# Optimization experiments

Hardware: AMD Instinct MI355X
Metric: run time of the kernel (lower is better)

Reference implementation:

```python
import jax, jax.numpy as jnp
import numpy as np

B = 512          # number of drug-combination graphs (batch)
MAX_LEN = 128    # static padding for to_dense_batch
D_DRUG = 256     # drug_in_features (kdim = vdim)
D_CELL = 1024    # cell_in_features
H = 16           # nheads
HD = 64          # h (per-head dim)
E = H * HD       # embed_dim = 1024


def setup_inputs() -> dict:
    key = jax.random.key(0)
    ks = jax.random.split(key, 12)
    N = 32768
    x_nodes = jax.random.normal(ks[0], (N, D_DRUG), dtype=jnp.float32)
    guide = jnp.sort(jax.random.randint(ks[1], (N,), 0, B)).astype(jnp.int64)
    cell = jax.random.normal(ks[2], (B, D_CELL), dtype=jnp.float32)
    s = 0.02
    return {
        "x_nodes": x_nodes,
        "cell": cell,
        "Wq": jax.random.normal(ks[3], (E, E), dtype=jnp.float32) * s,
        "bq": jnp.zeros((E,), dtype=jnp.float32),
        "Wk": jax.random.normal(ks[4], (E, D_DRUG), dtype=jnp.float32) * s,
        "bk": jnp.zeros((E,), dtype=jnp.float32),
        "Wv": jax.random.normal(ks[5], (E, D_DRUG), dtype=jnp.float32) * s,
        "bv": jnp.zeros((E,), dtype=jnp.float32),
        "Wo": jax.random.normal(ks[6], (E, E), dtype=jnp.float32) * s,
        "bo": jnp.zeros((E,), dtype=jnp.float32),
        "Wc": jax.random.normal(ks[7], (E, D_CELL), dtype=jnp.float32) * s,
        "bc": jnp.zeros((E,), dtype=jnp.float32),
        "guide": guide,
    }


def _to_dense_batch(x_nodes, guide):
    # Faithful torch_geometric.to_dense_batch with static MAX_LEN padding.
    N = x_nodes.shape[0]
    ones = jnp.ones((N,), dtype=jnp.int32)
    counts = jax.ops.segment_sum(ones, guide, num_segments=B)      # [B]
    starts = jnp.cumsum(counts) - counts                            # [B]
    pos = jnp.arange(N, dtype=jnp.int32) - starts[guide]            # rank within segment
    dense = jnp.zeros((B, MAX_LEN, x_nodes.shape[1]), x_nodes.dtype).at[guide, pos].set(x_nodes)
    mask = jnp.zeros((B, MAX_LEN), dtype=bool).at[guide, pos].set(True)
    return dense, mask


def reference(x_nodes, cell, Wq, bq, Wk, bk, Wv, bv, Wo, bo, Wc, bc, guide):
    drug_key, mask = _to_dense_batch(x_nodes, guide)                # [B,M,D_DRUG], [B,M]
    # cell_query_fc then MHA q-projection (single query per graph)
    cq = cell @ Wc.T + bc                                           # [B,E]
    q = (cq @ Wq.T + bq).reshape(B, H, HD) * (HD ** -0.5)           # [B,H,hd]
    k = (drug_key @ Wk.T + bk).reshape(B, MAX_LEN, H, HD)           # [B,M,H,hd]
    v = (drug_key @ Wv.T + bv).reshape(B, MAX_LEN, H, HD)
    scores = jnp.einsum('bhd,bmhd->bhm', q, k)                      # [B,H,M]
    scores = jnp.where(mask[:, None, :], scores, -1e9)
    attn = jax.nn.softmax(scores, axis=-1)
    out = jnp.einsum('bhm,bmhd->bhd', attn, v).reshape(B, E)        # [B,E]
    out = out @ Wo.T + bo
    return jnp.concatenate([out, cell], axis=1)                     # [B, E + D_CELL]
```

## Files before the change

### kernel.cpp

```cpp
#include <hip/hip_runtime.h>
#include <hip/hip_bf16.h>
#include <math.h>

#define B_GRAPHS 512
#define MAXLEN   128
#define DDRUG    256
#define NH       16
#define EMB      1024

typedef __attribute__((ext_vector_type(4))) float f32x4;
typedef __attribute__((ext_vector_type(8))) short s16x8;
typedef __attribute__((ext_vector_type(4))) short s16x4;

__device__ inline short f2bf(float f) {
    unsigned u = __builtin_bit_cast(unsigned, f);
    u += 0x7FFF + ((u >> 16) & 1);
    return (short)(u >> 16);
}
__device__ inline float bf2f(short s) {
    unsigned u = ((unsigned)(unsigned short)s) << 16;
    return __builtin_bit_cast(float, u);
}

__device__ inline void cvt4(const float* __restrict__ in, short* __restrict__ out, int j)
{
    f32x4 v = ((const f32x4*)in)[j];
    s16x4 o;
    o.x = f2bf(v.x); o.y = f2bf(v.y); o.z = f2bf(v.z); o.w = f2bf(v.w);
    ((s16x4*)out)[j] = o;
}

__global__ __launch_bounds__(256) void prep_kernel(
    const float* __restrict__ cell, const float* __restrict__ Wc,
    const float* __restrict__ Wq,   const float* __restrict__ Wo,
    const float* __restrict__ Wv,   const int* __restrict__ g32, int N,
    float* __restrict__ out, short* __restrict__ cell_bf, short* __restrict__ Wc_bf,
    short* __restrict__ Wq_bf, short* __restrict__ Wo_bf, short* __restrict__ Wv_bf,
    int* __restrict__ starts)
{
    const int stride = gridDim.x * 256;
    for (int i = blockIdx.x * 256 + threadIdx.x; i < 1114625; i += stride) {
        if      (i <  131072) cvt4(cell, cell_bf, i);
        else if (i <  393216) cvt4(Wc, Wc_bf, i - 131072);
        else if (i <  655360) cvt4(Wq, Wq_bf, i - 393216);
        else if (i <  917504) cvt4(Wo, Wo_bf, i - 655360);
        else if (i <  983040) cvt4(Wv, Wv_bf, i - 917504);
        else if (i < 1114112) {
            int j = i - 983040;
            int b = j >> 8, c4 = j & 255;
            *(f32x4*)&out[(size_t)b * 2048 + 1024 + c4 * 4] = ((const f32x4*)cell)[j];
        } else {
            int b = i - 1114112;
            bool is64 = (g32[N - 1] == 0);
            int lo = 0, hi = N;
            while (lo < hi) {
                int mid = (lo + hi) >> 1;
                int v = is64 ? g32[2 * mid] : g32[mid];
                if (v < b) lo = mid + 1; else hi = mid;
            }
            starts[b] = lo;
        }
    }
}

template<bool OUT_BF>
__global__ __launch_bounds__(256) void gemm32_bf16_nt(
    const short* __restrict__ A, int lda,
    const short* __restrict__ Bw, int ldb,
    const float* __restrict__ bias, void* __restrict__ Cout,
    int ldc, float scale, int K)
{
    __shared__ short As[32 * 64];
    __shared__ short Bs[32 * 64];
    const int t = threadIdx.x, lane = t & 63, w = t >> 6;
    const int wm = w >> 1, wn = w & 1;
    const int row0 = blockIdx.y * 32, col0 = blockIdx.x * 32;
    f32x4 c = {0.f, 0.f, 0.f, 0.f};

    const int sr = t >> 3, sc = (t & 7) * 8;
    const int swz = (sr & 7) << 4;

    for (int kt = 0; kt < K; kt += 64) {
        s16x8 va = *(const s16x8*)&A [(size_t)(row0 + sr) * lda + kt + sc];
        s16x8 vb = *(const s16x8*)&Bw[(size_t)(col0 + sr) * ldb + kt + sc];
        *(s16x8*)((char*)As + sr * 128 + ((sc * 2) ^ swz)) = va;
        *(s16x8*)((char*)Bs + sr * 128 + ((sc * 2) ^ swz)) = vb;
        __syncthreads();
        #pragma unroll
        for (int ks = 0; ks < 2; ++ks) {
            const int kk = (ks * 32 + (lane >> 4) * 8) * 2;
            int ra = wm * 16 + (lane & 15);
            s16x8 a = *(const s16x8*)((char*)As + ra * 128 + (kk ^ ((ra & 7) << 4)));
            int rb = wn * 16 + (lane & 15);
            s16x8 b = *(const s16x8*)((char*)Bs + rb * 128 + (kk ^ ((rb & 7) << 4)));
            c = __builtin_amdgcn_mfma_f32_16x16x32_bf16(a, b, c, 0, 0, 0);
        }
        __syncthreads();
    }
    const int m0 = row0 + wm * 16 + (lane >> 4) * 4;
    const int nn = col0 + wn * 16 + (lane & 15);
    #pragma unroll
    for (int r = 0; r < 4; ++r) {
        float v = (c[r] + bias[nn]) * scale;
        if (OUT_BF) ((short*)Cout)[(size_t)(m0 + r) * ldc + nn] = f2bf(v);
        else        ((float*)Cout)[(size_t)(m0 + r) * ldc + nn] = v;
    }
}

__global__ __launch_bounds__(256) void qk_kernel(
    const float* __restrict__ q, const float* __restrict__ Wk, short* __restrict__ qkout)
{
    __shared__ float q_s[8][64];
    const int bt = blockIdx.x, h = blockIdx.y, t = threadIdx.x;
    for (int i = t; i < 512; i += 256)
        q_s[i >> 6][i & 63] = q[(size_t)(bt * 8 + (i >> 6)) * EMB + h * 64 + (i & 63)];
    __syncthreads();
    float acc[8] = {};
    const float* wbase = &Wk[(size_t)h * 64 * DDRUG + t];
    #pragma unroll 4
    for (int j = 0; j < 64; ++j) {
        float wv = wbase[(size_t)j * DDRUG];
        #pragma unroll
        for (int bb = 0; bb < 8; ++bb) acc[bb] += q_s[bb][j] * wv;
    }
    #pragma unroll
    for (int bb = 0; bb < 8; ++bb)
        qkout[(size_t)(bt * 8 + bb) * 4096 + h * DDRUG + t] = f2bf(acc[bb]);
}

__global__ __launch_bounds__(256) void attn_kernel(
    const float* __restrict__ X, const short* __restrict__ qk,
    const int* __restrict__ starts, short* __restrict__ xbar, int Ntot)
{
    __shared__ short qk_s[8 * 256];
    __shared__ short Xs[64 * 256];
    __shared__ float S_s[128 * 12];
    const int b = blockIdx.x, half = blockIdx.y, t = threadIdx.x;
    const int lane = t & 63, w = t >> 6;
    const int s0 = starts[b];
    int n = starts[b + 1] - s0;
    if (n > MAXLEN) n = MAXLEN;

    {
        int hl = t >> 5, cc = (t & 31) * 8;
        const s16x8* src = (const s16x8*)(qk + (size_t)b * 4096 + (half * 8 + hl) * 256 + cc);
        *(s16x8*)((char*)qk_s + hl * 512 + ((cc * 2) ^ ((hl & 7) << 4))) = src[0];
    }

    const int sr = t >> 2, scg = (t & 3) * 64;
    auto stageX = [&](int st) {
        int gm = s0 + st * 64 + sr;
        if (gm > Ntot - 1) gm = Ntot - 1;
        const f32x4* src = (const f32x4*)(X + (size_t)gm * 256 + scg);
        int swzr = (sr & 7) << 4;
        #pragma unroll
        for (int j = 0; j < 8; ++j) {
            f32x4 a = src[2 * j], bb = src[2 * j + 1];
            s16x8 v;
            v[0] = f2bf(a.x);  v[1] = f2bf(a.y);  v[2] = f2bf(a.z);  v[3] = f2bf(a.w);
            v[4] = f2bf(bb.x); v[5] = f2bf(bb.y); v[6] = f2bf(bb.z); v[7] = f2bf(bb.w);
            *(s16x8*)((char*)Xs + sr * 512 + (((scg + j * 8) * 2) ^ swzr)) = v;
        }
    };
    stageX(0);
    __syncthreads();

    s16x8 af[8];
    {
        int r = lane & 7, swzh = r << 4;
        #pragma unroll
        for (int ks = 0; ks < 8; ++ks) {
            int k = ks * 32 + (lane >> 4) * 8;
            af[ks] = *(const s16x8*)((char*)qk_s + r * 512 + ((k * 2) ^ swzh));
        }
    }
    auto mfmaStage = [&](int st) {
        int lr = w * 16 + (lane & 15);
        int swzr = (lr & 7) << 4;
        f32x4 c = {0.f, 0.f, 0.f, 0.f};
        #pragma unroll
        for (int ks = 0; ks < 8; ++ks) {
            int k = ks * 32 + (lane >> 4) * 8;
            s16x8 bf = *(const s16x8*)((char*)Xs + lr * 512 + ((k * 2) ^ swzr));
            c = __builtin_amdgcn_mfma_f32_16x16x32_bf16(af[ks], bf, c, 0, 0, 0);
        }
        int m = st * 64 + w * 16 + (lane & 15);
        int hb = (lane >> 4) * 4;
        if (hb < 8) {
            #pragma unroll
            for (int i = 0; i < 4; ++i) S_s[m * 12 + hb + i] = c[i];
        }
    };
    mfmaStage(0);
    if (n > 64) {
        __syncthreads();
        stageX(1);
        __syncthreads();
        mfmaStage(1);
    }
    __syncthreads();

    #pragma unroll
    for (int hh = 0; hh < 2; ++hh) {
        int h = w * 2 + hh;
        float v0 = (lane < n)      ? S_s[lane * 12 + h]        : -INFINITY;
        float v1 = (lane + 64 < n) ? S_s[(lane + 64) * 12 + h] : -INFINITY;
        float mx = fmaxf(v0, v1);
        #pragma unroll
        for (int off = 32; off > 0; off >>= 1) mx = fmaxf(mx, __shfl_xor(mx, off, 64));
        float e0 = (lane < n)      ? __expf(v0 - mx) : 0.f;
        float e1 = (lane + 64 < n) ? __expf(v1 - mx) : 0.f;
        float sm = e0 + e1;
        #pragma unroll
        for (int off = 32; off > 0; off >>= 1) sm += __shfl_xor(sm, off, 64);
        float inv = 1.f / sm;
        if (lane < n)      S_s[lane * 12 + h]        = e0 * inv;
        if (lane + 64 < n) S_s[(lane + 64) * 12 + h] = e1 * inv;
    }
    __syncthreads();

    const int d = t;
    float acc[8] = {};
    const float* Xb = X + (size_t)s0 * 256 + d;
    int m = 0;
    for (; m + 4 <= n; m += 4) {
        float xv[4];
        #pragma unroll
        for (int u = 0; u < 4; ++u) xv[u] = Xb[(size_t)(m + u) * 256];
        #pragma unroll
        for (int u = 0; u < 4; ++u) {
            const f32x4* prow = (const f32x4*)&S_s[(m + u) * 12];
            f32x4 p0 = prow[0], p1 = prow[1];
            float x = xv[u];
            acc[0] += p0.x * x; acc[1] += p0.y * x; acc[2] += p0.z * x; acc[3] += p0.w * x;
            acc[4] += p1.x * x; acc[5] += p1.y * x; acc[6] += p1.z * x; acc[7] += p1.w * x;
        }
    }
    for (; m < n; ++m) {
        const f32x4* prow = (const f32x4*)&S_s[m * 12];
        f32x4 p0 = prow[0], p1 = prow[1];
        float x = Xb[(size_t)m * 256];
        acc[0] += p0.x * x; acc[1] += p0.y * x; acc[2] += p0.z * x; acc[3] += p0.w * x;
        acc[4] += p1.x * x; acc[5] += p1.y * x; acc[6] += p1.z * x; acc[7] += p1.w * x;
    }
    short* xb = xbar + (size_t)b * 4096 + (size_t)(half * 8) * 256 + d;
    #pragma unroll
    for (int h = 0; h < 8; ++h) xb[(size_t)h * 256] = f2bf(acc[h]);
}

__global__ __launch_bounds__(256) void outh_gemm(
    const short* __restrict__ xbar,
    const short* __restrict__ Wv_bf,
    const float* __restrict__ bv, short* __restrict__ outh)
{
    __shared__ short As[64 * 64];
    __shared__ short Bs[64 * 64];
    const int t = threadIdx.x, lane = t & 63, w = t >> 6;
    const int wm = w >> 1, wn = w & 1;
    const int h = blockIdx.y;
    const int row0 = blockIdx.x * 64;
    const short* A = xbar + (size_t)h * 256;
    const short* B = Wv_bf + (size_t)h * 64 * 256;
    f32x4 c[2][2] = {};

    const int sr = t >> 2, sc = (t & 3) * 16;
    const int swz = (sr & 7) << 4;
    const int kb0 = (lane >> 4) * 8;

    for (int kt = 0; kt < 256; kt += 64) {
        s16x8 va0 = *(const s16x8*)&A[(size_t)(row0 + sr) * 4096 + kt + sc];
        s16x8 va1 = *(const s16x8*)&A[(size_t)(row0 + sr) * 4096 + kt + sc + 8];
        s16x8 vb0 = *(const s16x8*)&B[(size_t)sr * 256 + kt + sc];
        s16x8 vb1 = *(const s16x8*)&B[(size_t)sr * 256 + kt + sc + 8];
        *(s16x8*)((char*)As + sr * 128 + ((sc * 2)      ^ swz)) = va0;
        *(s16x8*)((char*)As + sr * 128 + ((sc * 2 + 16) ^ swz)) = va1;
        *(s16x8*)((char*)Bs + sr * 128 + ((sc * 2)      ^ swz)) = vb0;
        *(s16x8*)((char*)Bs + sr * 128 + ((sc * 2 + 16) ^ swz)) = vb1;
        __syncthreads();
        #pragma unroll
        for (int ks = 0; ks < 2; ++ks) {
            const int kk = (ks * 32 + kb0) * 2;
            s16x8 a0, a1, b0, b1;
            {
                int r = wm * 32 + (lane & 15);
                a0 = *(const s16x8*)((char*)As + r * 128 + (kk ^ ((r & 7) << 4)));
                int r2 = r + 16;
                a1 = *(const s16x8*)((char*)As + r2 * 128 + (kk ^ ((r2 & 7) << 4)));
            }
            {
                int r = wn * 32 + (lane & 15);
                b0 = *(const s16x8*)((char*)Bs + r * 128 + (kk ^ ((r & 7) << 4)));
                int r2 = r + 16;
                b1 = *(const s16x8*)((char*)Bs + r2 * 128 + (kk ^ ((r2 & 7) << 4)));
            }
            c[0][0] = __builtin_amdgcn_mfma_f32_16x16x32_bf16(a0, b0, c[0][0], 0, 0, 0);
            c[0][1] = __builtin_amdgcn_mfma_f32_16x16x32_bf16(a0, b1, c[0][1], 0, 0, 0);
            c[1][0] = __builtin_amdgcn_mfma_f32_16x16x32_bf16(a1, b0, c[1][0], 0, 0, 0);
            c[1][1] = __builtin_amdgcn_mfma_f32_16x16x32_bf16(a1, b1, c[1][1], 0, 0, 0);
        }
        __syncthreads();
    }
    #pragma unroll
    for (int i = 0; i < 2; ++i)
    #pragma unroll
    for (int j = 0; j < 2; ++j) {
        int m0 = row0 + wm * 32 + i * 16 + (lane >> 4) * 4;
        int nn = wn * 32 + j * 16 + (lane & 15);
        #pragma unroll
        for (int r = 0; r < 4; ++r) {
            float v = c[i][j][r] + bv[h * 64 + nn];
            outh[(size_t)(m0 + r) * EMB + h * 64 + nn] = f2bf(v);
        }
    }
}

extern "C" void kernel_launch(void* const* d_in, const int* in_sizes, int n_in,
                              void* d_out, int out_size, void* d_ws, size_t ws_size,
                              hipStream_t stream)
{
    const float* x_nodes = (const float*)d_in[0];
    const float* cell    = (const float*)d_in[1];
    const float* Wq      = (const float*)d_in[2];
    const float* bq      = (const float*)d_in[3];
    const float* Wk      = (const float*)d_in[4];
    const float* Wv      = (const float*)d_in[6];
    const float* bv      = (const float*)d_in[7];
    const float* Wo      = (const float*)d_in[8];
    const float* bo      = (const float*)d_in[9];
    const float* Wc      = (const float*)d_in[10];
    const float* bc      = (const float*)d_in[11];
    const int*   guide   = (const int*)d_in[12];
    const int N = in_sizes[12];
    float* out = (float*)d_out;

    char* ws = (char*)d_ws;
    int*   starts  = (int*)ws;
    float* qf32    = (float*)(ws + 4096);
    short* cell_bf = (short*)(ws + 4096 + (2u << 20));
    short* cq_bf   = (short*)(ws + 4096 + (3u << 20));
    short* outh_bf = (short*)(ws + 4096 + (4u << 20));
    short* qk_bf   = (short*)(ws + 4096 + (5u << 20));
    short* xbar_bf = (short*)(ws + 4096 + (9u << 20));
    short* Wc_bf   = (short*)(ws + 4096 + (13u << 20));
    short* Wq_bf   = (short*)(ws + 4096 + (15u << 20));
    short* Wo_bf   = (short*)(ws + 4096 + (17u << 20));
    short* Wv_bf   = (short*)(ws + 4096 + (19u << 20));

    prep_kernel<<<2048, 256, 0, stream>>>(
        cell, Wc, Wq, Wo, Wv, guide, N, out,
        cell_bf, Wc_bf, Wq_bf, Wo_bf, Wv_bf, starts);

    gemm32_bf16_nt<true ><<<dim3(32, 16), 256, 0, stream>>>(
        cell_bf, 1024, Wc_bf, 1024, bc, cq_bf, 1024, 1.0f, 1024);
    gemm32_bf16_nt<false><<<dim3(32, 16), 256, 0, stream>>>(
        cq_bf, 1024, Wq_bf, 1024, bq, qf32, 1024, 0.125f, 1024);

    qk_kernel<<<dim3(B_GRAPHS / 8, NH), 256, 0, stream>>>(qf32, Wk, qk_bf);

    attn_kernel<<<dim3(B_GRAPHS, 2), 256, 0, stream>>>(x_nodes, qk_bf, starts, xbar_bf, N);

    outh_gemm<<<dim3(8, NH), 256, 0, stream>>>(xbar_bf, Wv_bf, bv, outh_bf);

    gemm32_bf16_nt<false><<<dim3(32, 16), 256, 0, stream>>>(
        outh_bf, 1024, Wo_bf, 1024, bo, out, 2048, 1.0f, 1024);

    (void)in_sizes; (void)n_in; (void)out_size; (void)ws_size;
}
```

Before: 181.4 us.

## Process all heads per graph block and reuse staged bf16 X for weighted sum

The attention kernel now handles all 16 heads in a single block per graph instead of splitting heads across two blocks. This halves the global reads of the fp32 node features X. The whole 128-row X tile is staged into shared memory as bf16, and the attention-weighted sum reads from that tile instead of re-reading fp32 X from global memory. In exchange the kernel uses more LDS (64KB X plus the score buffer), which lowers occupancy, launches half as many blocks, and now accumulates the weighted sum from bf16-rounded X.

```diff
diff --git a/kernel.cpp b/kernel.cpp
--- a/kernel.cpp
+++ b/kernel.cpp
@@ -132,24 +132,25 @@
     const float* __restrict__ X, const short* __restrict__ qk,
     const int* __restrict__ starts, short* __restrict__ xbar, int Ntot)
 {
-    __shared__ short qk_s[8 * 256];
-    __shared__ short Xs[64 * 256];
-    __shared__ float S_s[128 * 12];
-    const int b = blockIdx.x, half = blockIdx.y, t = threadIdx.x;
+    __shared__ short Xs[128 * 256];
+    __shared__ float S_s[128 * 20];
+    const int b = blockIdx.x, t = threadIdx.x;
     const int lane = t & 63, w = t >> 6;
     const int s0 = starts[b];
     int n = starts[b + 1] - s0;
     if (n > MAXLEN) n = MAXLEN;
 
+    s16x8 af[8];
     {
-        int hl = t >> 5, cc = (t & 31) * 8;
-        const s16x8* src = (const s16x8*)(qk + (size_t)b * 4096 + (half * 8 + hl) * 256 + cc);
-        *(s16x8*)((char*)qk_s + hl * 512 + ((cc * 2) ^ ((hl & 7) << 4))) = src[0];
+        const short* qb = qk + (size_t)b * 4096 + (lane & 15) * 256 + (lane >> 4) * 8;
+        #pragma unroll
+        for (int ks = 0; ks < 8; ++ks) af[ks] = *(const s16x8*)(qb + ks * 32);
     }
 
     const int sr = t >> 2, scg = (t & 3) * 64;
     auto stageX = [&](int st) {
-        int gm = s0 + st * 64 + sr;
+        int lrow = st * 64 + sr;
+        int gm = s0 + lrow;
         if (gm > Ntot - 1) gm = Ntot - 1;
         const f32x4* src = (const f32x4*)(X + (size_t)gm * 256 + scg);
         int swzr = (sr & 7) << 4;
@@ -159,23 +160,11 @@
             s16x8 v;
             v[0] = f2bf(a.x);  v[1] = f2bf(a.y);  v[2] = f2bf(a.z);  v[3] = f2bf(a.w);
             v[4] = f2bf(bb.x); v[5] = f2bf(bb.y); v[6] = f2bf(bb.z); v[7] = f2bf(bb.w);
-            *(s16x8*)((char*)Xs + sr * 512 + (((scg + j * 8) * 2) ^ swzr)) = v;
+            *(s16x8*)((char*)Xs + lrow * 512 + (((scg + j * 8) * 2) ^ swzr)) = v;
         }
     };
-    stageX(0);
-    __syncthreads();
-
-    s16x8 af[8];
-    {
-        int r = lane & 7, swzh = r << 4;
-        #pragma unroll
-        for (int ks = 0; ks < 8; ++ks) {
-            int k = ks * 32 + (lane >> 4) * 8;
-            af[ks] = *(const s16x8*)((char*)qk_s + r * 512 + ((k * 2) ^ swzh));
-        }
-    }
     auto mfmaStage = [&](int st) {
-        int lr = w * 16 + (lane & 15);
+        int lr = st * 64 + w * 16 + (lane & 15);
         int swzr = (lr & 7) << 4;
         f32x4 c = {0.f, 0.f, 0.f, 0.f};
         #pragma unroll
@@ -184,27 +173,26 @@
             s16x8 bf = *(const s16x8*)((char*)Xs + lr * 512 + ((k * 2) ^ swzr));
             c = __builtin_amdgcn_mfma_f32_16x16x32_bf16(af[ks], bf, c, 0, 0, 0);
         }
-        int m = st * 64 + w * 16 + (lane & 15);
         int hb = (lane >> 4) * 4;
-        if (hb < 8) {
-            #pragma unroll
-            for (int i = 0; i < 4; ++i) S_s[m * 12 + hb + i] = c[i];
-        }
+        #pragma unroll
+        for (int i = 0; i < 4; ++i) S_s[lr * 20 + hb + i] = c[i];
     };
+
+    stageX(0);
+    __syncthreads();
+    if (n > 64) stageX(1);
     mfmaStage(0);
     if (n > 64) {
         __syncthreads();
-        stageX(1);
-        __syncthreads();
         mfmaStage(1);
     }
     __syncthreads();
 
     #pragma unroll
-    for (int hh = 0; hh < 2; ++hh) {
-        int h = w * 2 + hh;
-        float v0 = (lane < n)      ? S_s[lane * 12 + h]        : -INFINITY;
-        float v1 = (lane + 64 < n) ? S_s[(lane + 64) * 12 + h] : -INFINITY;
+    for (int hh = 0; hh < 4; ++hh) {
+        int h = w * 4 + hh;
+        float v0 = (lane < n)      ? S_s[lane * 20 + h]        : -INFINITY;
+        float v1 = (lane + 64 < n) ? S_s[(lane + 64) * 20 + h] : -INFINITY;
         float mx = fmaxf(v0, v1);
         #pragma unroll
         for (int off = 32; off > 0; off >>= 1) mx = fmaxf(mx, __shfl_xor(mx, off, 64));
@@ -214,38 +202,26 @@
         #pragma unroll
         for (int off = 32; off > 0; off >>= 1) sm += __shfl_xor(sm, off, 64);
         float inv = 1.f / sm;
-        if (lane < n)      S_s[lane * 12 + h]        = e0 * inv;
-        if (lane + 64 < n) S_s[(lane + 64) * 12 + h] = e1 * inv;
+        if (lane < n)      S_s[lane * 20 + h]        = e0 * inv;
+        if (lane + 64 < n) S_s[(lane + 64) * 20 + h] = e1 * inv;
     }
     __syncthreads();
 
     const int d = t;
-    float acc[8] = {};
-    const float* Xb = X + (size_t)s0 * 256 + d;
-    int m = 0;
-    for (; m + 4 <= n; m += 4) {
-        float xv[4];
-        #pragma unroll
-        for (int u = 0; u < 4; ++u) xv[u] = Xb[(size_t)(m + u) * 256];
-        #pragma unroll
-        for (int u = 0; u < 4; ++u) {
-            const f32x4* prow = (const f32x4*)&S_s[(m + u) * 12];
-            f32x4 p0 = prow[0], p1 = prow[1];
-            float x = xv[u];
-            acc[0] += p0.x * x; acc[1] += p0.y * x; acc[2] += p0.z * x; acc[3] += p0.w * x;
-            acc[4] += p1.x * x; acc[5] += p1.y * x; acc[6] += p1.z * x; acc[7] += p1.w * x;
-        }
-    }
-    for (; m < n; ++m) {
-        const f32x4* prow = (const f32x4*)&S_s[m * 12];
-        f32x4 p0 = prow[0], p1 = prow[1];
-        float x = Xb[(size_t)m * 256];
-        acc[0] += p0.x * x; acc[1] += p0.y * x; acc[2] += p0.z * x; acc[3] += p0.w * x;
-        acc[4] += p1.x * x; acc[5] += p1.y * x; acc[6] += p1.z * x; acc[7] += p1.w * x;
-    }
-    short* xb = xbar + (size_t)b * 4096 + (size_t)(half * 8) * 256 + d;
-    #pragma unroll
-    for (int h = 0; h < 8; ++h) xb[(size_t)h * 256] = f2bf(acc[h]);
+    float acc[16] = {};
+    #pragma unroll 2
+    for (int m = 0; m < n; ++m) {
+        float x = bf2f(*(const short*)((char*)Xs + m * 512 + ((2 * d) ^ ((m & 7) << 4))));
+        const f32x4* prow = (const f32x4*)&S_s[m * 20];
+        f32x4 p0 = prow[0], p1 = prow[1], p2 = prow[2], p3 = prow[3];
+        acc[0]  += p0.x * x; acc[1]  += p0.y * x; acc[2]  += p0.z * x; acc[3]  += p0.w * x;
+        acc[4]  += p1.x * x; acc[5]  += p1.y * x; acc[6]  += p1.z * x; acc[7]  += p1.w * x;
+        acc[8]  += p2.x * x; acc[9]  += p2.y * x; acc[10] += p2.z * x; acc[11] += p2.w * x;
+        acc[12] += p3.x * x; acc[13] += p3.y * x; acc[14] += p3.z * x; acc[15] += p3.w * x;
+    }
+    short* xb = xbar + (size_t)b * 4096 + d;
+    #pragma unroll
+    for (int h = 0; h < 16; ++h) xb[(size_t)h * 256] = f2bf(acc[h]);
 }
 
 __global__ __launch_bounds__(256) void outh_gemm(
@@ -357,7 +333,7 @@
 
     qk_kernel<<<dim3(B_GRAPHS / 8, NH), 256, 0, stream>>>(qf32, Wk, qk_bf);
 
-    attn_kernel<<<dim3(B_GRAPHS, 2), 256, 0, stream>>>(x_nodes, qk_bf, starts, xbar_bf, N);
+    attn_kernel<<<B_GRAPHS, 256, 0, stream>>>(x_nodes, qk_bf, starts, xbar_bf, N);
 
     outh_gemm<<<dim3(8, NH), 256, 0, stream>>>(xbar_bf, Wv_bf, bv, outh_bf);
 
```

Result: faster. 169.8 us (-6.4%).
